# Kernel optimization log

Hardware: AMD Instinct MI355X
Metric: run time of the kernel (lower is better)

## Reference

```python
import jax, jax.numpy as jnp
import numpy as np

B, S, D, H, MRP = 2, 2048, 1024, 16, 128
DK = D // H
NUM_REL = 2 * MRP + 1


def setup_inputs() -> dict:
    key = jax.random.key(0)
    ks = jax.random.split(key, 14)
    w = lambda k, shp: (jax.random.normal(k, shp, jnp.float32) * 0.02)
    return {
        'query': jax.random.normal(ks[0], (B, S, D), jnp.float32),
        'key':   jax.random.normal(ks[1], (B, S, D), jnp.float32),
        'value': jax.random.normal(ks[2], (B, S, D), jnp.float32),
        'Wq': w(ks[3], (D, D)), 'bq': jnp.zeros((D,), jnp.float32),
        'Wk': w(ks[4], (D, D)), 'bk': jnp.zeros((D,), jnp.float32),
        'Wv': w(ks[5], (D, D)), 'bv': jnp.zeros((D,), jnp.float32),
        'Wo': w(ks[6], (D, D)), 'bo': jnp.zeros((D,), jnp.float32),
        'rel_k': w(ks[7], (NUM_REL, DK)),
        'rel_v': w(ks[8], (NUM_REL, DK)),
    }


def reference(query, key, value, Wq, bq, Wk, bk, Wv, bv, Wo, bo, rel_k, rel_v):
    b, s, d = query.shape
    h, dk = H, DK
    # projections -> (b, h, s, dk)
    Q = (query @ Wq.T + bq).reshape(b, s, h, dk).transpose(0, 2, 1, 3)
    K = (key   @ Wk.T + bk).reshape(b, s, h, dk).transpose(0, 2, 1, 3)
    V = (value @ Wv.T + bv).reshape(b, s, h, dk).transpose(0, 2, 1, 3)
    # relative position indices: distance(i,j) = j - i, clipped, shifted to [0, 2*MRP]
    pos = jnp.arange(s)
    rel_idx = jnp.clip(pos[None, :] - pos[:, None], -MRP, MRP) + MRP  # (s, s)
    rk = rel_k[rel_idx]  # (s, s, dk)
    rv = rel_v[rel_idx]  # (s, s, dk)
    # content scores + relative-key scores
    scores = jnp.einsum('bhqd,bhkd->bhqk', Q, K)
    scores = scores + jnp.einsum('bhqd,qkd->bhqk', Q, rk)
    scores = scores * (1.0 / np.sqrt(dk).astype(np.float32))
    attn = jax.nn.softmax(scores, axis=-1)  # (b, h, s, s)
    # content context + relative-value context
    ctx = jnp.einsum('bhqk,bhkd->bhqd', attn, V)
    ctx = ctx + jnp.einsum('bhqk,qkd->bhqd', attn, rv)
    ctx = ctx.transpose(0, 2, 1, 3).reshape(b, s, d)
    out = ctx @ Wo.T + bo
    return out, attn
```

## Files before the change

kernel.cpp:

```cpp
#include <hip/hip_runtime.h>
#include <hip/hip_bf16.h>
#include <cstdint>
#include <cstddef>

using u16 = unsigned short;
using u32 = unsigned int;

typedef float f32x4 __attribute__((ext_vector_type(4)));
typedef short s16x8 __attribute__((ext_vector_type(8)));
typedef _Float16 f16x8 __attribute__((ext_vector_type(8)));
typedef unsigned short u16x4 __attribute__((ext_vector_type(4)));
typedef u32 u32x4 __attribute__((ext_vector_type(4)));

constexpr int Bc  = 2;
constexpr int Sc  = 2048;
constexpr int Dc  = 1024;
constexpr int Hc  = 16;
constexpr int DKc = 64;
constexpr int BHc = Bc * Hc;
constexpr int NREL = 257;
constexpr int RKROWS = 272;
constexpr int RVCOLS = 288;

constexpr float QSCALE = 0.125f * 1.4426950408889634f;

__device__ __forceinline__ u16 f2bf(float x){
  return __builtin_bit_cast(u16, __float2bfloat16(x));
}
__device__ __forceinline__ float bf2f(u16 u){
  return __builtin_bit_cast(float, (u32)u << 16);
}
__device__ __forceinline__ u16 f2h(float x){
  return __builtin_bit_cast(u16, (_Float16)x);
}
__device__ __forceinline__ u32 packh2(float a, float b){
  u16 x = __builtin_bit_cast(u16, (_Float16)a);
  u16 y = __builtin_bit_cast(u16, (_Float16)b);
  return (u32)x | ((u32)y << 16);
}
__device__ __forceinline__ float h2f_lo(u32 w){
  return (float)__builtin_bit_cast(_Float16, (u16)(w & 0xffffu));
}
__device__ __forceinline__ float h2f_hi(u32 w){
  return (float)__builtin_bit_cast(_Float16, (u16)(w >> 16));
}
__device__ __forceinline__ f32x4 mfma16(s16x8 a, s16x8 b, f32x4 c){
  return __builtin_amdgcn_mfma_f32_16x16x32_bf16(a, b, c, 0, 0, 0);
}
__device__ __forceinline__ f32x4 mfma16h(f16x8 a, f16x8 b, f32x4 c){
  return __builtin_amdgcn_mfma_f32_16x16x32_f16(a, b, c, 0, 0, 0);
}
__device__ __forceinline__ s16x8 ld8(const u16* p){
  return *reinterpret_cast<const s16x8*>(p);
}
__device__ __forceinline__ f16x8 ld8h(const u16* p){
  return *reinterpret_cast<const f16x8*>(p);
}
__device__ __forceinline__ void st_bf8(u16* p, float4 a, float4 b){
  s16x8 t;
  t[0] = (short)f2bf(a.x); t[1] = (short)f2bf(a.y);
  t[2] = (short)f2bf(a.z); t[3] = (short)f2bf(a.w);
  t[4] = (short)f2bf(b.x); t[5] = (short)f2bf(b.y);
  t[6] = (short)f2bf(b.z); t[7] = (short)f2bf(b.w);
  *reinterpret_cast<s16x8*>(p) = t;
}

__global__ void prep_rel(const float* __restrict__ rel_k,
                         const float* __restrict__ rel_v,
                         u16* __restrict__ relkb, u16* __restrict__ relvT)
{
  int tid = blockIdx.x * blockDim.x + threadIdx.x;
  int nthr = gridDim.x * blockDim.x;
  for (int i = tid; i < RKROWS * DKc; i += nthr){
    int r = i >> 6, c = i & 63;
    float v = (r < NREL) ? rel_k[r * DKc + c] : 0.0f;
    relkb[i] = f2bf(v);
  }
  for (int i = tid; i < DKc * RVCOLS; i += nthr){
    int d = i / RVCOLS, j = i - d * RVCOLS;
    float v = (j < NREL) ? rel_v[j * DKc + d] : 0.0f;
    relvT[i] = f2h(v);
  }
}

__global__ __launch_bounds__(256, 4) void proj_gemm(
    const float* __restrict__ Xq, const float* __restrict__ Xk, const float* __restrict__ Xv,
    const float* __restrict__ Wq, const float* __restrict__ Wk, const float* __restrict__ Wv,
    const float* __restrict__ bq, const float* __restrict__ bk, const float* __restrict__ bv,
    u16* __restrict__ Qb, u16* __restrict__ Kb, u16* __restrict__ Vt)
{
  const int type = blockIdx.y;
  const float* X    = (type == 0) ? Xq : (type == 1) ? Xk : Xv;
  const float* W    = (type == 0) ? Wq : (type == 1) ? Wk : Wv;
  const float* bias = (type == 0) ? bq : (type == 1) ? bk : bv;

  const int m0 = (int)(blockIdx.x >> 4) * 64;
  const int n0 = (int)(blockIdx.x & 15) * 64;

  __shared__ alignas(16) u16 As[64][56];
  __shared__ alignas(16) u16 Bs[64][56];

  const int tid  = threadIdx.x;
  const int wid  = tid >> 6, lane = tid & 63;
  const int lgrp = lane >> 4, lidx = lane & 15;
  const int wr   = wid >> 1,  wc   = wid & 1;

  const int srow = tid >> 2;
  const int scol = (tid & 3) << 3;

  f32x4 acc[2][2] = {};

  for (int it = 0; it < Dc / 32; ++it){
    const int k0 = it * 32;
    const float* xa = &X[(size_t)(m0 + srow) * Dc + k0 + scol];
    const float* xb = &W[(size_t)(n0 + srow) * Dc + k0 + scol];
    float4 a0 = *reinterpret_cast<const float4*>(xa);
    float4 a1 = *reinterpret_cast<const float4*>(xa + 4);
    float4 b0 = *reinterpret_cast<const float4*>(xb);
    float4 b1 = *reinterpret_cast<const float4*>(xb + 4);
    __syncthreads();
    st_bf8(&As[srow][scol], a0, a1);
    st_bf8(&Bs[srow][scol], b0, b1);
    __syncthreads();
    s16x8 af0 = ld8(&As[wr * 32 + lidx][lgrp * 8]);
    s16x8 af1 = ld8(&As[wr * 32 + 16 + lidx][lgrp * 8]);
    s16x8 bf0 = ld8(&Bs[wc * 32 + lidx][lgrp * 8]);
    s16x8 bf1 = ld8(&Bs[wc * 32 + 16 + lidx][lgrp * 8]);
    acc[0][0] = mfma16(af0, bf0, acc[0][0]);
    acc[0][1] = mfma16(af0, bf1, acc[0][1]);
    acc[1][0] = mfma16(af1, bf0, acc[1][0]);
    acc[1][1] = mfma16(af1, bf1, acc[1][1]);
  }

#pragma unroll
  for (int fm = 0; fm < 2; ++fm)
#pragma unroll
    for (int fn = 0; fn < 2; ++fn)
#pragma unroll
      for (int r = 0; r < 4; ++r){
        int mRow = m0 + wr * 32 + fm * 16 + lgrp * 4 + r;
        int nCol = n0 + wc * 32 + fn * 16 + lidx;
        float v = acc[fm][fn][r] + bias[nCol];
        int b = mRow >> 11, s = mRow & (Sc - 1);
        int h = nCol >> 6,  dk = nCol & 63;
        int bh = b * Hc + h;
        if (type == 0)      Qb[((size_t)bh * Sc + s) * DKc + dk] = f2bf(v * QSCALE);
        else if (type == 1) Kb[((size_t)bh * Sc + s) * DKc + dk] = f2bf(v);
        else                Vt[((size_t)bh * DKc + dk) * Sc + s] = f2h(v);
      }
}

__global__ __launch_bounds__(512, 4) void attn_fused(
    const u16* __restrict__ Qb, const u16* __restrict__ Kb, const u16* __restrict__ Vt,
    const u16* __restrict__ relkb, const u16* __restrict__ relvT,
    float* __restrict__ attn_out, u16* __restrict__ ctxb)
{
  __shared__ alignas(16) char smem[51904];
  u32*  Pw        = reinterpret_cast<u32*>(smem);
  u16 (*Rld)[260] = reinterpret_cast<u16(*)[260]>(smem + 32768);
  u16 (*Ag)[288]  = reinterpret_cast<u16(*)[288]>(smem + 41088);
  float* red      = reinterpret_cast<float*>(smem + 50304);
  float* rscRow   = reinterpret_cast<float*>(smem + 51840);
  float (*ctxS)[16][64] = reinterpret_cast<float(*)[16][64]>(smem);

  const int tid  = threadIdx.x;
  const int wid  = tid >> 6, lane = tid & 63;
  const int lgrp = lane >> 4, lidx = lane & 15;

  const int flat    = (int)blockIdx.x;
  const int logical = (flat & 7) * 512 + (flat >> 3);
  const int bh      = logical >> 7;
  const int qtile   = logical & 127;
  const int q0      = qtile * 16;
  const int kbase   = wid * 256;

  const u16* Qp = Qb + (size_t)bh * Sc * DKc;
  const u16* Kp = Kb + (size_t)bh * Sc * DKc;
  const u16* Vp = Vt + (size_t)bh * DKc * Sc;
  float* attp   = attn_out + (size_t)bh * Sc * Sc;

  s16x8 aq0 = ld8(&Qp[(size_t)(q0 + lidx) * DKc + lgrp * 8]);
  s16x8 aq1 = ld8(&Qp[(size_t)(q0 + lidx) * DKc + 32 + lgrp * 8]);

  for (int jt = wid; jt < 17; jt += 8){
    int j0 = jt * 16;
    s16x8 b0 = ld8(&relkb[(size_t)(j0 + lidx) * DKc + lgrp * 8]);
    s16x8 b1 = ld8(&relkb[(size_t)(j0 + lidx) * DKc + 32 + lgrp * 8]);
    f32x4 rr = {0.f, 0.f, 0.f, 0.f};
    rr = mfma16(aq0, b0, rr);
    rr = mfma16(aq1, b1, rr);
    int j = j0 + lidx;
    if (j <= 256){
#pragma unroll
      for (int t = 0; t < 4; ++t) Rld[lgrp * 4 + t][j] = f2bf(rr[t]);
    }
  }
  {
    u32* agp = reinterpret_cast<u32*>(&Ag[0][0]);
    for (int i = tid; i < 16 * 288 / 2; i += 512) agp[i] = 0u;
  }
  __syncthreads();

  const float RloL = bf2f(Rld[lidx][0]);
  const float RhiL = bf2f(Rld[lidx][256]);
  const int kperm = ((lidx >> 2) << 3) + (lidx & 3);

  u32x4 pw[8];
  f32x4 cacc[4] = {};
  float l = 0.f, clow = 0.f, chigh = 0.f;

#pragma unroll
  for (int kb = 0; kb < 8; ++kb){
    const int kO = kbase + kb * 32;
    const bool all_lo = (kO + 31 - q0) <= -128;
    const bool all_hi = (kO - (q0 + 15)) >= 128;
    const u16* kr = &Kp[(size_t)(kO + kperm) * DKc];
    s16x8 bk00 = ld8(kr + lgrp * 8);
    s16x8 bk01 = ld8(kr + 32 + lgrp * 8);
    s16x8 bk10 = ld8(kr + 4 * DKc + lgrp * 8);
    s16x8 bk11 = ld8(kr + 4 * DKc + 32 + lgrp * 8);
    f16x8 bv0 = ld8h(&Vp[(size_t)(lidx) * Sc + kO + lgrp * 8]);
    f16x8 bv1 = ld8h(&Vp[(size_t)(16 + lidx) * Sc + kO + lgrp * 8]);
    f16x8 bv2 = ld8h(&Vp[(size_t)(32 + lidx) * Sc + kO + lgrp * 8]);
    f16x8 bv3 = ld8h(&Vp[(size_t)(48 + lidx) * Sc + kO + lgrp * 8]);

    f32x4 a0 = {0.f, 0.f, 0.f, 0.f}, a1 = {0.f, 0.f, 0.f, 0.f};
    a0 = mfma16(bk00, aq0, a0); a0 = mfma16(bk01, aq1, a0);
    a1 = mfma16(bk10, aq0, a1); a1 = mfma16(bk11, aq1, a1);

    float pu[8];
    if (all_lo | all_hi){
      const float addv = all_lo ? RloL : RhiL;
#pragma unroll
      for (int j = 0; j < 4; ++j){
        pu[j]     = __builtin_amdgcn_exp2f(a0[j] + addv);
        pu[j + 4] = __builtin_amdgcn_exp2f(a1[j] + addv);
      }
      float ps = ((pu[0] + pu[1]) + (pu[2] + pu[3])) + ((pu[4] + pu[5]) + (pu[6] + pu[7]));
      if (all_lo) clow += ps; else chigh += ps;
      l += ps;
    } else {
      const int dd0 = kO + lgrp * 8 - (q0 + lidx);
#pragma unroll
      for (int j = 0; j < 8; ++j){
        int dd = dd0 + j;
        float add = (dd <= -128) ? RloL : (dd >= 128) ? RhiL : bf2f(Rld[lidx][dd + 128]);
        float av = (j < 4) ? a0[j] : a1[j - 4];
        float p = __builtin_amdgcn_exp2f(av + add);
        pu[j] = p;
        if (dd <= -128)      clow  += p;
        else if (dd >= 128)  chigh += p;
        else                 Ag[lidx][dd + 128] = f2h(p);
      }
      l += ((pu[0] + pu[1]) + (pu[2] + pu[3])) + ((pu[4] + pu[5]) + (pu[6] + pu[7]));
    }
    u32x4 w4 = {packh2(pu[0], pu[1]), packh2(pu[2], pu[3]),
                packh2(pu[4], pu[5]), packh2(pu[6], pu[7])};
    pw[kb] = w4;
    f16x8 ap = __builtin_bit_cast(f16x8, w4);
    cacc[0] = mfma16h(ap, bv0, cacc[0]);
    cacc[1] = mfma16h(ap, bv1, cacc[1]);
    cacc[2] = mfma16h(ap, bv2, cacc[2]);
    cacc[3] = mfma16h(ap, bv3, cacc[3]);
  }

  l     += __shfl_xor(l, 16);      l     += __shfl_xor(l, 32);
  clow  += __shfl_xor(clow, 16);   clow  += __shfl_xor(clow, 32);
  chigh += __shfl_xor(chigh, 16);  chigh += __shfl_xor(chigh, 32);
  if (lane < 16){
    red[wid * 16 + lidx]       = l;
    red[128 + wid * 16 + lidx] = clow;
    red[256 + wid * 16 + lidx] = chigh;
  }
  __syncthreads();
  if (tid < 16){
    float s = 0.f, cl = 0.f, ch = 0.f;
#pragma unroll
    for (int w = 0; w < 8; ++w){
      s  += red[w * 16 + tid];
      cl += red[128 + w * 16 + tid];
      ch += red[256 + w * 16 + tid];
    }
    rscRow[tid] = 1.0f / s;
    Ag[tid][0]   = f2h(cl);
    Ag[tid][256] = f2h(ch);
  }
  __syncthreads();

  {
    u32* PwW = Pw + wid * 1024;
    const int xsw = (lidx & 7) << 2;
#pragma unroll
    for (int h = 0; h < 2; ++h){
#pragma unroll
      for (int kb4 = 0; kb4 < 4; ++kb4){
        int csw = (kb4 * 16 + lgrp * 4) ^ xsw;
        *reinterpret_cast<u32x4*>(&PwW[lidx * 64 + csw]) = pw[h * 4 + kb4];
      }
      __asm__ volatile("" ::: "memory");
#pragma unroll
      for (int rr = 0; rr < 8; ++rr){
        const int row = rr * 2 + (lane >> 5);
        const int cc  = ((lane & 31) * 2) ^ ((row & 7) << 2);
        u32 w0 = PwW[row * 64 + cc];
        u32 w1 = PwW[row * 64 + cc + 1];
        float sc_ = rscRow[row];
        f32x4 o;
        o[0] = h2f_lo(w0) * sc_;
        o[1] = h2f_hi(w0) * sc_;
        o[2] = h2f_lo(w1) * sc_;
        o[3] = h2f_hi(w1) * sc_;
        __builtin_nontemporal_store(o, reinterpret_cast<f32x4*>(
            &attp[(size_t)(q0 + row) * Sc + kbase + h * 128 + (lane & 31) * 4]));
      }
      __asm__ volatile("" ::: "memory");
    }
  }

  for (int t = wid; t < 9; t += 8){
    const int j0 = t * 32;
    f16x8 aa = ld8h(&Ag[lidx][j0 + lgrp * 8]);
#pragma unroll
    for (int dg = 0; dg < 4; ++dg){
      f16x8 bb = ld8h(&relvT[(size_t)(dg * 16 + lidx) * RVCOLS + j0 + lgrp * 8]);
      cacc[dg] = mfma16h(aa, bb, cacc[dg]);
    }
  }
#pragma unroll
  for (int dg = 0; dg < 4; ++dg)
#pragma unroll
    for (int r = 0; r < 4; ++r) cacc[dg][r] *= rscRow[lgrp * 4 + r];

  __syncthreads();

#pragma unroll
  for (int dg = 0; dg < 4; ++dg)
#pragma unroll
    for (int r = 0; r < 4; ++r)
      ctxS[wid][lgrp * 4 + r][dg * 16 + lidx] = cacc[dg][r];
  __syncthreads();

  if (tid < 256){
    const int row2 = tid >> 4, qd = tid & 15;
    f32x4 sum = {0.f, 0.f, 0.f, 0.f};
#pragma unroll
    for (int w = 0; w < 8; ++w)
      sum += *reinterpret_cast<f32x4*>(&ctxS[w][row2][qd * 4]);
    const int b = bh >> 4, h = bh & 15;
    u16x4 o;
#pragma unroll
    for (int i = 0; i < 4; ++i) o[i] = f2bf(sum[i]);
    *reinterpret_cast<u16x4*>(&ctxb[((size_t)(b * Sc + q0 + row2)) * Dc + h * 64 + qd * 4]) = o;
  }
}

__global__ __launch_bounds__(256, 4) void out_gemm(
    const u16* __restrict__ A, const float* __restrict__ W,
    const float* __restrict__ bias, float* __restrict__ out)
{
  const int m0 = (int)(blockIdx.x >> 4) * 64;
  const int n0 = (int)(blockIdx.x & 15) * 64;

  __shared__ alignas(16) u16 As[64][56];
  __shared__ alignas(16) u16 Bs[64][56];

  const int tid  = threadIdx.x;
  const int wid  = tid >> 6, lane = tid & 63;
  const int lgrp = lane >> 4, lidx = lane & 15;
  const int wr   = wid >> 1,  wc   = wid & 1;
  const int srow = tid >> 2;
  const int scol = (tid & 3) << 3;

  f32x4 acc[2][2] = {};

  for (int it = 0; it < Dc / 32; ++it){
    const int k0 = it * 32;
    s16x8 av = ld8(&A[(size_t)(m0 + srow) * Dc + k0 + scol]);
    const float* xb = &W[(size_t)(n0 + srow) * Dc + k0 + scol];
    float4 b0 = *reinterpret_cast<const float4*>(xb);
    float4 b1 = *reinterpret_cast<const float4*>(xb + 4);
    __syncthreads();
    *reinterpret_cast<s16x8*>(&As[srow][scol]) = av;
    st_bf8(&Bs[srow][scol], b0, b1);
    __syncthreads();
    s16x8 af0 = ld8(&As[wr * 32 + lidx][lgrp * 8]);
    s16x8 af1 = ld8(&As[wr * 32 + 16 + lidx][lgrp * 8]);
    s16x8 bf0 = ld8(&Bs[wc * 32 + lidx][lgrp * 8]);
    s16x8 bf1 = ld8(&Bs[wc * 32 + 16 + lidx][lgrp * 8]);
    acc[0][0] = mfma16(af0, bf0, acc[0][0]);
    acc[0][1] = mfma16(af0, bf1, acc[0][1]);
    acc[1][0] = mfma16(af1, bf0, acc[1][0]);
    acc[1][1] = mfma16(af1, bf1, acc[1][1]);
  }

#pragma unroll
  for (int fm = 0; fm < 2; ++fm)
#pragma unroll
    for (int fn = 0; fn < 2; ++fn)
#pragma unroll
      for (int r = 0; r < 4; ++r){
        int mRow = m0 + wr * 32 + fm * 16 + lgrp * 4 + r;
        int nCol = n0 + wc * 32 + fn * 16 + lidx;
        out[(size_t)mRow * Dc + nCol] = acc[fm][fn][r] + bias[nCol];
      }
}

extern "C" void kernel_launch(void* const* d_in, const int* in_sizes, int n_in,
                              void* d_out, int out_size, void* d_ws, size_t ws_size,
                              hipStream_t stream)
{
  const float* query = (const float*)d_in[0];
  const float* key_  = (const float*)d_in[1];
  const float* value = (const float*)d_in[2];
  const float* Wq    = (const float*)d_in[3];
  const float* bq    = (const float*)d_in[4];
  const float* Wk    = (const float*)d_in[5];
  const float* bk    = (const float*)d_in[6];
  const float* Wv    = (const float*)d_in[7];
  const float* bv    = (const float*)d_in[8];
  const float* Wo    = (const float*)d_in[9];
  const float* bo    = (const float*)d_in[10];
  const float* rel_k = (const float*)d_in[11];
  const float* rel_v = (const float*)d_in[12];

  float* outp  = (float*)d_out;
  float* attnp = outp + (size_t)Bc * Sc * Dc;

  u16* Qb    = (u16*)d_ws;
  u16* Kb    = Qb + (size_t)BHc * Sc * DKc;
  u16* Vt    = Kb + (size_t)BHc * Sc * DKc;
  u16* ctxb  = Vt + (size_t)BHc * Sc * DKc;
  u16* relkb = ctxb + (size_t)Bc * Sc * Dc;
  u16* relvT = relkb + (size_t)RKROWS * DKc;

  prep_rel<<<dim3(32), dim3(256), 0, stream>>>(rel_k, rel_v, relkb, relvT);
  proj_gemm<<<dim3((Bc * Sc / 64) * (Dc / 64), 3), dim3(256), 0, stream>>>(
      query, key_, value, Wq, Wk, Wv, bq, bk, bv, Qb, Kb, Vt);
  attn_fused<<<dim3((Sc / 16) * BHc), dim3(512), 0, stream>>>(
      Qb, Kb, Vt, relkb, relvT, attnp, ctxb);
  out_gemm<<<dim3((Bc * Sc / 64) * (Dc / 64)), dim3(256), 0, stream>>>(
      ctxb, Wo, bo, outp);
}
```

Before: 392.4 us.

## Shrink attention LDS footprint to raise occupancy with serialized ctx reduction

Cuts the fused attention kernel's shared memory from about 51 KB to about 23 KB and raises the launch-bounds minimum blocks per CU from 4 to 8. To fit, the per-wave P staging buffer is halved and drained in four 64-column chunks. The relative-value MFMA is moved before the attn store so the staging area can overlay other buffers. The per-wave ctx partials are now accumulated into a single 16x64 buffer in eight serialized passes. This adds eight barriers and may force register spilling under the tighter launch bound.

```diff
diff --git a/kernel.cpp b/kernel.cpp
--- a/kernel.cpp
+++ b/kernel.cpp
@@ -150,18 +150,18 @@
       }
 }
 
-__global__ __launch_bounds__(512, 4) void attn_fused(
+__global__ __launch_bounds__(512, 8) void attn_fused(
     const u16* __restrict__ Qb, const u16* __restrict__ Kb, const u16* __restrict__ Vt,
     const u16* __restrict__ relkb, const u16* __restrict__ relvT,
     float* __restrict__ attn_out, u16* __restrict__ ctxb)
 {
-  __shared__ alignas(16) char smem[51904];
-  u32*  Pw        = reinterpret_cast<u32*>(smem);
-  u16 (*Rld)[260] = reinterpret_cast<u16(*)[260]>(smem + 32768);
-  u16 (*Ag)[288]  = reinterpret_cast<u16(*)[288]>(smem + 41088);
-  float* red      = reinterpret_cast<float*>(smem + 50304);
-  float* rscRow   = reinterpret_cast<float*>(smem + 51840);
-  float (*ctxS)[16][64] = reinterpret_cast<float(*)[16][64]>(smem);
+  __shared__ alignas(16) char smem[23232];
+  u16 (*Rld)[260]   = reinterpret_cast<u16(*)[260]>(smem);
+  u16 (*Ag)[288]    = reinterpret_cast<u16(*)[288]>(smem + 8320);
+  float* red        = reinterpret_cast<float*>(smem + 17536);
+  float* rscRow     = reinterpret_cast<float*>(smem + 19072);
+  float (*ctxS)[64] = reinterpret_cast<float(*)[64]>(smem + 19136);
+  u32*  Pw          = reinterpret_cast<u32*>(smem);
 
   const int tid  = threadIdx.x;
   const int wid  = tid >> 6, lane = tid & 63;
@@ -287,23 +287,39 @@
   }
   __syncthreads();
 
+  for (int t = wid; t < 9; t += 8){
+    const int j0 = t * 32;
+    f16x8 aa = ld8h(&Ag[lidx][j0 + lgrp * 8]);
+#pragma unroll
+    for (int dg = 0; dg < 4; ++dg){
+      f16x8 bb = ld8h(&relvT[(size_t)(dg * 16 + lidx) * RVCOLS + j0 + lgrp * 8]);
+      cacc[dg] = mfma16h(aa, bb, cacc[dg]);
+    }
+  }
+#pragma unroll
+  for (int dg = 0; dg < 4; ++dg)
+#pragma unroll
+    for (int r = 0; r < 4; ++r) cacc[dg][r] *= rscRow[lgrp * 4 + r];
+
+  __syncthreads();
+
   {
-    u32* PwW = Pw + wid * 1024;
+    u32* PwW = Pw + wid * 512;
     const int xsw = (lidx & 7) << 2;
 #pragma unroll
-    for (int h = 0; h < 2; ++h){
-#pragma unroll
-      for (int kb4 = 0; kb4 < 4; ++kb4){
-        int csw = (kb4 * 16 + lgrp * 4) ^ xsw;
-        *reinterpret_cast<u32x4*>(&PwW[lidx * 64 + csw]) = pw[h * 4 + kb4];
+    for (int qt = 0; qt < 4; ++qt){
+#pragma unroll
+      for (int b = 0; b < 2; ++b){
+        int csw = (b * 16 + lgrp * 4) ^ xsw;
+        *reinterpret_cast<u32x4*>(&PwW[lidx * 32 + csw]) = pw[qt * 2 + b];
       }
       __asm__ volatile("" ::: "memory");
 #pragma unroll
-      for (int rr = 0; rr < 8; ++rr){
-        const int row = rr * 2 + (lane >> 5);
-        const int cc  = ((lane & 31) * 2) ^ ((row & 7) << 2);
-        u32 w0 = PwW[row * 64 + cc];
-        u32 w1 = PwW[row * 64 + cc + 1];
+      for (int i = 0; i < 4; ++i){
+        const int row = (lane >> 3) + 8 * (i >> 1);
+        const int c0  = (((lane & 7) * 2 + (i & 1) * 16)) ^ ((row & 7) << 2);
+        u32 w0 = PwW[row * 32 + c0];
+        u32 w1 = PwW[row * 32 + c0 + 1];
         float sc_ = rscRow[row];
         f32x4 o;
         o[0] = h2f_lo(w0) * sc_;
@@ -311,41 +327,29 @@
         o[2] = h2f_lo(w1) * sc_;
         o[3] = h2f_hi(w1) * sc_;
         __builtin_nontemporal_store(o, reinterpret_cast<f32x4*>(
-            &attp[(size_t)(q0 + row) * Sc + kbase + h * 128 + (lane & 31) * 4]));
+            &attp[(size_t)(q0 + row) * Sc + kbase + qt * 64 + (i & 1) * 32 + (lane & 7) * 4]));
       }
       __asm__ volatile("" ::: "memory");
     }
   }
 
-  for (int t = wid; t < 9; t += 8){
-    const int j0 = t * 32;
-    f16x8 aa = ld8h(&Ag[lidx][j0 + lgrp * 8]);
-#pragma unroll
-    for (int dg = 0; dg < 4; ++dg){
-      f16x8 bb = ld8h(&relvT[(size_t)(dg * 16 + lidx) * RVCOLS + j0 + lgrp * 8]);
-      cacc[dg] = mfma16h(aa, bb, cacc[dg]);
-    }
-  }
-#pragma unroll
-  for (int dg = 0; dg < 4; ++dg)
-#pragma unroll
-    for (int r = 0; r < 4; ++r) cacc[dg][r] *= rscRow[lgrp * 4 + r];
-
-  __syncthreads();
-
-#pragma unroll
-  for (int dg = 0; dg < 4; ++dg)
-#pragma unroll
-    for (int r = 0; r < 4; ++r)
-      ctxS[wid][lgrp * 4 + r][dg * 16 + lidx] = cacc[dg][r];
-  __syncthreads();
+  for (int w = 0; w < 8; ++w){
+    if (wid == w){
+#pragma unroll
+      for (int dg = 0; dg < 4; ++dg)
+#pragma unroll
+        for (int r = 0; r < 4; ++r){
+          const int row = lgrp * 4 + r, col = dg * 16 + lidx;
+          if (w == 0) ctxS[row][col] = cacc[dg][r];
+          else        ctxS[row][col] += cacc[dg][r];
+        }
+    }
+    __syncthreads();
+  }
 
   if (tid < 256){
     const int row2 = tid >> 4, qd = tid & 15;
-    f32x4 sum = {0.f, 0.f, 0.f, 0.f};
-#pragma unroll
-    for (int w = 0; w < 8; ++w)
-      sum += *reinterpret_cast<f32x4*>(&ctxS[w][row2][qd * 4]);
+    f32x4 sum = *reinterpret_cast<f32x4*>(&ctxS[row2][qd * 4]);
     const int b = bh >> 4, h = bh & 15;
     u16x4 o;
 #pragma unroll
```

Result: slower. 649.6 us (+65.5%).
